# Kernel optimization log

Measured on AMD Instinct MI355X. Metric: run time of the kernel, lower is better.

Reference implementation:

```python
import jax, jax.numpy as jnp
from jax import lax
import numpy as np

IN_F, CELL, OUT_F = 1024, 1024, 1024
B, T = 128, 256


def setup_inputs() -> dict:
    key = jax.random.key(0)
    ks = jax.random.split(key, 12)
    s_gate = 1.0 / np.sqrt(IN_F + CELL)
    s_cls = 1.0 / np.sqrt(CELL)
    d = {
        "x": jax.random.normal(ks[0], (B, T, IN_F), jnp.float32),
        "Wf": jax.random.normal(ks[1], (CELL + IN_F, CELL), jnp.float32) * s_gate,
        "bf": jax.random.normal(ks[2], (CELL,), jnp.float32) * s_gate,
        "Wi1": jax.random.normal(ks[3], (CELL + IN_F, CELL), jnp.float32) * s_gate,
        "bi1": jax.random.normal(ks[4], (CELL,), jnp.float32) * s_gate,
        "Wi2": jax.random.normal(ks[5], (CELL + IN_F, CELL), jnp.float32) * s_gate,
        "bi2": jax.random.normal(ks[6], (CELL,), jnp.float32) * s_gate,
        "Wo": jax.random.normal(ks[7], (CELL + IN_F, CELL), jnp.float32) * s_gate,
        "bo": jax.random.normal(ks[8], (CELL,), jnp.float32) * s_gate,
        "Wc": jax.random.normal(ks[9], (CELL, OUT_F), jnp.float32) * s_cls,
        "bc": jax.random.normal(ks[10], (OUT_F,), jnp.float32) * s_cls,
    }
    return d


def reference(x, Wf, bf, Wi1, bi1, Wi2, bi2, Wo, bo, Wc, bc):
    # x: [B, T, IN_F]
    Bsz, Tlen, _ = x.shape
    H = Wf.shape[1]
    xt = jnp.transpose(x, (1, 0, 2))  # [T, B, IN_F], matches x.permute(1,0,2)

    def step(cell, x_i):
        # concat order matches torch.cat((cell_state, x[i]), dim=2)
        inp = jnp.concatenate([cell, x_i], axis=-1)  # [B, H + IN_F]
        f = jax.nn.sigmoid(inp @ Wf + bf)
        cell1 = cell * f
        i1 = jax.nn.sigmoid(inp @ Wi1 + bi1)
        i2 = jnp.tanh(inp @ Wi2 + bi2)
        cell2 = cell1 + i1 * i2
        o1 = jax.nn.sigmoid(inp @ Wo + bo)
        h = o1 * jnp.tanh(cell2)
        out = h @ Wc + bc  # [B, OUT_F]
        return cell2, out

    c0 = jnp.zeros((Bsz, H), x.dtype)
    c_final, outs = lax.scan(step, c0, xt)  # outs: [T, B, OUT_F]
    output_sequence = jnp.transpose(outs, (1, 0, 2))  # [B, T, OUT_F]
    return output_sequence, c_final[None, :, :]  # cell_state kept as [1, B, H]
```

## Files before the change

### kernel.cpp

```cpp
#include <hip/hip_runtime.h>
#include <cstdint>
#include <cstddef>

#define DEVINL __device__ __forceinline__

typedef __attribute__((ext_vector_type(8))) short bf16x8;
typedef __attribute__((ext_vector_type(4))) float f32x4;
typedef __attribute__((ext_vector_type(4))) unsigned short u16x4;
typedef __attribute__((ext_vector_type(4))) unsigned int u32x4;

static constexpr size_t OFF_XB   = 0;
static constexpr size_t OFF_WHT  = OFF_XB  + (size_t)32768*1024*2;
static constexpr size_t OFF_WXT  = OFF_WHT + (size_t)4096*1024*2;
static constexpr size_t OFF_WCT  = OFF_WXT + (size_t)4096*1024*2;
static constexpr size_t OFF_BIAS = OFF_WCT + (size_t)1024*1024*2;
static constexpr size_t OFF_XW   = OFF_BIAS + 4096*4;
static constexpr size_t OFF_H    = OFF_XW  + (size_t)32768*4096*2;
static constexpr size_t OFF_CB   = OFF_H   + (size_t)32768*1024*2;
static constexpr size_t OFF_BAR  = OFF_CB  + (size_t)2*128*1024*2;
static constexpr size_t WS_NEEDED = OFF_BAR + 32768;

DEVINL unsigned short f2b(float f) {
  union { float f; unsigned u; } v; v.f = f;
  unsigned r = (v.u + 0x7FFFu + ((v.u >> 16) & 1u)) >> 16;
  return (unsigned short)r;
}
DEVINL float b2f(unsigned short h) {
  union { unsigned u; float f; } v; v.u = ((unsigned)h) << 16;
  return v.f;
}
DEVINL float sigmoidf_(float x) { return 1.0f / (1.0f + __expf(-x)); }
DEVINL float tanhf_(float x) { float e = __expf(2.0f * x); return 1.0f - 2.0f / (e + 1.0f); }
DEVINL f32x4 MFMA(bf16x8 a, bf16x8 b, f32x4 c) {
  return __builtin_amdgcn_mfma_f32_16x16x32_bf16(a, b, c, 0, 0, 0);
}
DEVINL void gload16(const void* g, void* l) {
  __builtin_amdgcn_global_load_lds(
      (const __attribute__((address_space(1))) void*)g,
      (__attribute__((address_space(3))) void*)l, 16, 0, 0);
}

__global__ void cvt_x_kernel(const float* __restrict__ x, unsigned short* __restrict__ xb) {
  size_t i = ((size_t)blockIdx.x * 256 + threadIdx.x) * 4;
  float4 v = *(const float4*)(x + i);
  u16x4 o; o.x = f2b(v.x); o.y = f2b(v.y); o.z = f2b(v.z); o.w = f2b(v.w);
  *(u16x4*)(xb + i) = o;
}

__global__ __launch_bounds__(256)
void cvt_w_kernel(const float* __restrict__ Wf, const float* __restrict__ Wi1,
                  const float* __restrict__ Wi2, const float* __restrict__ Wo,
                  unsigned short* __restrict__ WhT, unsigned short* __restrict__ WxT) {
  __shared__ float tile[64][65];
  const int bid = blockIdx.x;
  const int g  = bid & 3;
  const int kt = (bid >> 2) & 15;
  const int jt = bid >> 6;
  const float* W = (g == 0) ? Wf : (g == 1) ? Wi1 : (g == 2) ? Wi2 : Wo;
  const int tid = threadIdx.x;
  const int jj  = tid & 63;
  const int kr  = tid >> 6;

  for (int h = 0; h < 2; ++h) {
    const float* Wb = W + (size_t)(h ? 1024 : 0) * 1024;
#pragma unroll
    for (int i = 0; i < 16; ++i) {
      int kl = i * 4 + kr;
      tile[kl][jj] = Wb[(size_t)(kt * 64 + kl) * 1024 + jt * 64 + jj];
    }
    __syncthreads();
    unsigned short* Out = h ? WxT : WhT;
    unsigned short* op  = Out + (size_t)(4 * (jt * 64 + jj) + g) * 1024 + kt * 64 + kr * 16;
#pragma unroll
    for (int q = 0; q < 4; ++q) {
      u16x4 v;
#pragma unroll
      for (int e = 0; e < 4; ++e)
        ((unsigned short*)&v)[e] = f2b(tile[kr * 16 + q * 4 + e][jj]);
      *(u16x4*)(op + q * 4) = v;
    }
    __syncthreads();
  }
}

__global__ void bias_kernel(const float* __restrict__ bf_, const float* __restrict__ bi1,
                            const float* __restrict__ bi2, const float* __restrict__ bo,
                            float* __restrict__ biasAll) {
  int gc = blockIdx.x * 256 + threadIdx.x;
  int j = gc >> 2, g = gc & 3;
  const float* bb = (g == 0) ? bf_ : (g == 1) ? bi1 : (g == 2) ? bi2 : bo;
  biasAll[gc] = bb[j];
}

__global__ void cvt_wc_kernel(const float* __restrict__ Wc, unsigned short* __restrict__ WcT) {
  int idx = blockIdx.x * 256 + threadIdx.x;
  int k = idx & 1023, n = idx >> 10;
  WcT[idx] = f2b(Wc[(size_t)k * 1024 + n]);
}

template<bool OUT_F32>
__global__ __launch_bounds__(512, 2)
void gemm_bt(const unsigned short* __restrict__ A,
             const unsigned short* __restrict__ Bt,
             const float* __restrict__ bias,
             void* __restrict__ C,
             int M, int N, int K) {
  __shared__ char sT[4][32768];
  const int tid  = threadIdx.x;
  const int lane = tid & 63;
  const int wid  = tid >> 6;
  const int wm   = (wid >> 2) * 128;
  const int wn   = (wid & 3) * 64;

  const int nwg = gridDim.x * gridDim.y;
  const int lin = blockIdx.y * gridDim.x + blockIdx.x;
  const int cpx = nwg >> 3;
  const int swz = (lin & 7) * cpx + (lin >> 3);
  const int m0  = (swz / gridDim.x) * 256;
  const int n0  = (swz % gridDim.x) * 256;

  const int nt = K >> 5;

  f32x4 acc[8][4];
#pragma unroll
  for (int i = 0; i < 8; ++i)
#pragma unroll
    for (int j = 0; j < 4; ++j) acc[i][j] = (f32x4){0.f, 0.f, 0.f, 0.f};

  auto stageA = [&](int kt, int buf) {
#pragma unroll
    for (int l = 0; l < 2; ++l) {
      int s = l * 512 + tid;
      int r = s >> 2, c = s & 3;
      int cg = c ^ ((r >> 1) & 3);
      gload16(A + (size_t)(m0 + r) * K + kt * 32 + cg * 8, sT[buf] + s * 16);
    }
  };
  auto stageB = [&](int kt, int buf) {
#pragma unroll
    for (int l = 0; l < 2; ++l) {
      int s = l * 512 + tid;
      int r = s >> 2, c = s & 3;
      int cg = c ^ ((r >> 1) & 3);
      gload16(Bt + (size_t)(n0 + r) * K + kt * 32 + cg * 8, sT[buf] + 16384 + s * 16);
    }
  };

  stageA(0, 0); stageB(0, 0);
  stageA(1, 1); stageB(1, 1);
  stageA(2, 2); stageB(2, 2);
  asm volatile("s_waitcnt vmcnt(8)" ::: "memory");
  __builtin_amdgcn_s_barrier();

  const int ch = lane >> 4;

#pragma unroll 1
  for (int g = 0; g < nt; ++g) {
    const int rb = g & 3;
    const char* ab = sT[rb];
    const char* bb = sT[rb] + 16384;

    bf16x8 bv[4], av[4];
#pragma unroll
    for (int ni = 0; ni < 4; ++ni) {
      int col = wn + ni * 16 + (lane & 15);
      bv[ni] = *(const bf16x8*)(bb + col * 64 + ((ch ^ ((col >> 1) & 3)) << 4));
    }
#pragma unroll
    for (int mi = 0; mi < 4; ++mi) {
      int row = wm + mi * 16 + (lane & 15);
      av[mi] = *(const bf16x8*)(ab + row * 64 + ((ch ^ ((row >> 1) & 3)) << 4));
    }
    if (g + 3 < nt) stageA(g + 3, (g + 3) & 3);
    __builtin_amdgcn_s_barrier();
    __builtin_amdgcn_s_setprio(1);
#pragma unroll
    for (int mi = 0; mi < 4; ++mi)
#pragma unroll
      for (int ni = 0; ni < 4; ++ni)
        acc[mi][ni] = MFMA(av[mi], bv[ni], acc[mi][ni]);
    __builtin_amdgcn_s_setprio(0);
    __builtin_amdgcn_s_barrier();

#pragma unroll
    for (int mi = 0; mi < 4; ++mi) {
      int row = wm + 64 + mi * 16 + (lane & 15);
      av[mi] = *(const bf16x8*)(ab + row * 64 + ((ch ^ ((row >> 1) & 3)) << 4));
    }
    if (g + 3 < nt) stageB(g + 3, (g + 3) & 3);
    __builtin_amdgcn_s_barrier();
    __builtin_amdgcn_s_setprio(1);
#pragma unroll
    for (int mi = 0; mi < 4; ++mi)
#pragma unroll
      for (int ni = 0; ni < 4; ++ni)
        acc[mi + 4][ni] = MFMA(av[mi], bv[ni], acc[mi + 4][ni]);
    __builtin_amdgcn_s_setprio(0);

    if (g <= nt - 4)      asm volatile("s_waitcnt vmcnt(8)" ::: "memory");
    else if (g == nt - 3) asm volatile("s_waitcnt vmcnt(4)" ::: "memory");
    else if (g == nt - 2) asm volatile("s_waitcnt vmcnt(0)" ::: "memory");
    __builtin_amdgcn_s_barrier();
  }

#pragma unroll
  for (int mi = 0; mi < 8; ++mi)
#pragma unroll
    for (int ni = 0; ni < 4; ++ni)
#pragma unroll
      for (int r = 0; r < 4; ++r) {
        int row = m0 + wm + mi * 16 + (lane >> 4) * 4 + r;
        int col = n0 + wn + ni * 16 + (lane & 15);
        float v = acc[mi][ni][r] + bias[col];
        if (OUT_F32) ((float*)C)[(size_t)row * N + col] = v;
        else ((unsigned short*)C)[(size_t)row * N + col] = f2b(v);
      }
}

__global__ __launch_bounds__(512, 2)
void lstm_persist(const unsigned short* __restrict__ WhT,
                  const unsigned short* __restrict__ XW,
                  unsigned short* __restrict__ H,
                  unsigned short* __restrict__ cB0,
                  unsigned short* __restrict__ cB1,
                  float* __restrict__ cellOut,
                  unsigned* __restrict__ bar) {
  __shared__ __align__(16) char  sA[16 * 2064];
  __shared__ __align__(16) float sP[16 * 132];

  const int tid  = threadIdx.x;
  const int lane = tid & 63;
  const int nh   = tid >> 6;
  const int wgid = blockIdx.x;
  const int mq   = wgid & 7;
  const int cs   = wgid >> 3;
  const int sg   = cs >> 2;

  unsigned* qc   = bar + mq * 64;
  unsigned* qf   = bar + 512 + mq * 64;
  unsigned* gcnt = bar + 1024 + (mq * 8 + sg) * 64;

  const int r0 = lane & 15;
  const int ch = lane >> 4;

  bf16x8 bfr[32];
  {
    const unsigned short* bp = WhT + (size_t)(cs * 128 + nh * 16 + r0) * 1024 + ch * 8;
#pragma unroll
    for (int ks = 0; ks < 32; ++ks)
      bfr[ks] = *(const volatile bf16x8*)(bp + ks * 32);
  }

  const int erow  = tid >> 5;
  const int ecol  = tid & 31;
  const int browg = mq * 16 + erow;
  float cf = 0.f;

  const unsigned short* xwp = XW + (size_t)browg * 256 * 4096 + cs * 128 + ecol * 4;
  unsigned* c0p = (unsigned*)(cB0 + (size_t)browg * 1024 + cs * 32 + ecol);
  unsigned* c1p = (unsigned*)(cB1 + (size_t)browg * 1024 + cs * 32 + ecol);
  unsigned* hp  = (unsigned*)(H + (size_t)browg * 256 * 1024 + cs * 32 + ecol);

  const int strow = tid >> 7;
  const int stcc  = tid & 127;

  u16x4 xw = *(const u16x4*)(xwp);

  for (int t = 0; t < 256; ++t) {
    const unsigned short* cinq = ((t & 1) ? cB1 : cB0) + (size_t)mq * 16 * 1024;

    u32x4 st[4];
#pragma unroll
    for (int it = 0; it < 4; ++it) {
      const void* p = cinq + (size_t)(it * 4 + strow) * 1024 + stcc * 8;
      asm volatile("global_load_dwordx4 %0, %1, off sc0 sc1"
                   : "=&v"(st[it]) : "v"(p) : "memory");
    }
    asm volatile("s_waitcnt vmcnt(0)" ::: "memory");
    __builtin_amdgcn_sched_barrier(0);
#pragma unroll
    for (int it = 0; it < 4; ++it) {
      int r = it * 4 + strow;
      *(u32x4*)&sA[r * 2064 + stcc * 16] = st[it];
    }
    __syncthreads();

    f32x4 acc = (f32x4){0.f, 0.f, 0.f, 0.f};
#pragma unroll
    for (int ks = 0; ks < 32; ++ks) {
      bf16x8 a0 = *(const bf16x8*)&sA[r0 * 2064 + (ch + ks * 4) * 16];
      acc = MFMA(a0, bfr[ks], acc);
    }

#pragma unroll
    for (int rr = 0; rr < 4; ++rr)
      sP[(ch * 4 + rr) * 132 + nh * 16 + r0] = acc[rr];
    __syncthreads();

    float4 g = *(const float4*)&sP[erow * 132 + ecol * 4];
    float pf = g.x + b2f((unsigned short)xw[0]);
    float pi = g.y + b2f((unsigned short)xw[1]);
    float pg = g.z + b2f((unsigned short)xw[2]);
    float f  = sigmoidf_(pf), i1 = sigmoidf_(pi), gg = tanhf_(pg);
    float c2 = cf * f + i1 * gg; cf = c2;

    unsigned cl = f2b(c2);
    unsigned chi = __shfl_down(cl, 1);
    if (!(lane & 1))
      __hip_atomic_store((t & 1) ? c0p : c1p, cl | (chi << 16),
                         __ATOMIC_RELAXED, __HIP_MEMORY_SCOPE_AGENT);

    __syncthreads();
    if (tid == 0) {
      unsigned tgt1 = 4u * (unsigned)(t + 1);
      unsigned tgt2 = 8u * (unsigned)(t + 1);
      unsigned n = __hip_atomic_fetch_add(gcnt, 1u, __ATOMIC_RELAXED,
                                          __HIP_MEMORY_SCOPE_AGENT);
      if (n == tgt1 - 1u) {
        unsigned m = __hip_atomic_fetch_add(qc, 1u, __ATOMIC_RELAXED,
                                            __HIP_MEMORY_SCOPE_AGENT);
        if (m == tgt2 - 1u)
          __hip_atomic_store(qf, (unsigned)(t + 1),
                             __ATOMIC_RELAXED, __HIP_MEMORY_SCOPE_AGENT);
      }
    }

    {
      float po = g.w + b2f((unsigned short)xw[3]);
      float h  = sigmoidf_(po) * tanhf_(c2);
      unsigned hl = f2b(h);
      unsigned hh = __shfl_down(hl, 1);
      if (!(lane & 1))
        *(hp + (size_t)t * 512) = hl | (hh << 16);
    }
    if (t < 255) xw = *(const u16x4*)(xwp + (size_t)(t + 1) * 4096);

    if (tid == 0) {
      while (__hip_atomic_load(qf, __ATOMIC_RELAXED, __HIP_MEMORY_SCOPE_AGENT)
             < (unsigned)(t + 1))
        __builtin_amdgcn_s_sleep(1);
    }
    __syncthreads();
  }

  cellOut[(size_t)browg * 1024 + cs * 32 + ecol] = cf;
}

extern "C" void kernel_launch(void* const* d_in, const int* in_sizes, int n_in,
                              void* d_out, int out_size, void* d_ws, size_t ws_size,
                              hipStream_t stream) {
  const float* x   = (const float*)d_in[0];
  const float* Wf  = (const float*)d_in[1];
  const float* bfv = (const float*)d_in[2];
  const float* Wi1 = (const float*)d_in[3];
  const float* bi1 = (const float*)d_in[4];
  const float* Wi2 = (const float*)d_in[5];
  const float* bi2 = (const float*)d_in[6];
  const float* Wo  = (const float*)d_in[7];
  const float* bo  = (const float*)d_in[8];
  const float* Wc  = (const float*)d_in[9];
  const float* bc  = (const float*)d_in[10];
  float* out = (float*)d_out;

  if (ws_size < WS_NEEDED) return;

  char* ws = (char*)d_ws;
  unsigned short* xb      = (unsigned short*)(ws + OFF_XB);
  unsigned short* WhT     = (unsigned short*)(ws + OFF_WHT);
  unsigned short* WxT     = (unsigned short*)(ws + OFF_WXT);
  unsigned short* WcT     = (unsigned short*)(ws + OFF_WCT);
  float*          biasAll = (float*)(ws + OFF_BIAS);
  unsigned short* XW      = (unsigned short*)(ws + OFF_XW);
  unsigned short* H       = (unsigned short*)(ws + OFF_H);
  unsigned short* cB0     = (unsigned short*)(ws + OFF_CB);
  unsigned short* cB1     = (unsigned short*)(ws + OFF_CB + (size_t)128 * 1024 * 2);
  unsigned*       barLn   = (unsigned*)(ws + OFF_BAR);
  float*          cellOut = out + (size_t)32768 * 1024;

  hipMemsetAsync(cB0, 0, (size_t)128 * 1024 * 2, stream);
  hipMemsetAsync(barLn, 0, 32768, stream);

  cvt_x_kernel <<<32768, 256, 0, stream>>>(x, xb);
  cvt_w_kernel <<< 1024, 256, 0, stream>>>(Wf, Wi1, Wi2, Wo, WhT, WxT);
  bias_kernel  <<<   16, 256, 0, stream>>>(bfv, bi1, bi2, bo, biasAll);
  cvt_wc_kernel<<< 4096, 256, 0, stream>>>(Wc, WcT);

  gemm_bt<false><<<dim3(16, 128), 512, 0, stream>>>(xb, WxT, biasAll, XW, 32768, 4096, 1024);

  {
    void* args[] = { (void*)&WhT, (void*)&XW, (void*)&H,
                     (void*)&cB0, (void*)&cB1, (void*)&cellOut, (void*)&barLn };
    hipLaunchCooperativeKernel(lstm_persist, dim3(256), dim3(512), args, 0u, stream);
  }

  gemm_bt<true><<<dim3(4, 128), 512, 0, stream>>>(H, WcT, bc, out, 32768, 1024, 1024);
}
```

Before: 1.337 ms.

## Replace LDS gate transpose with in-register quad shuffles and split MFMA accumulators

The persistent recurrent kernel no longer writes MFMA gate results to shared memory and re-reads them after a barrier. Instead, each thread redistributes the four gate pre-activations inside its quad using lane shuffles, with thread-to-cell mapping changed to match. This removes one __syncthreads and the LDS round-trip from every timestep of the serial critical path. The MFMA chain is also split into four independent accumulators to break the dependency chain. In exchange it adds select/shuffle instructions and changes the h/c store pattern to stride-4 lane pairing.

```diff
diff --git a/kernel.cpp b/kernel.cpp
--- a/kernel.cpp
+++ b/kernel.cpp
@@ -225,8 +225,7 @@
                   unsigned short* __restrict__ cB1,
                   float* __restrict__ cellOut,
                   unsigned* __restrict__ bar) {
-  __shared__ __align__(16) char  sA[16 * 2064];
-  __shared__ __align__(16) float sP[16 * 132];
+  __shared__ __align__(16) char sA[16 * 2064];
 
   const int tid  = threadIdx.x;
   const int lane = tid & 63;
@@ -242,6 +241,8 @@
 
   const int r0 = lane & 15;
   const int ch = lane >> 4;
+  const int qq = r0 >> 2;
+  const int g  = r0 & 3;
 
   bf16x8 bfr[32];
   {
@@ -251,15 +252,14 @@
       bfr[ks] = *(const volatile bf16x8*)(bp + ks * 32);
   }
 
-  const int erow  = tid >> 5;
-  const int ecol  = tid & 31;
-  const int browg = mq * 16 + erow;
+  const int browg = mq * 16 + ch * 4 + g;
+  const int ccol  = cs * 32 + nh * 4 + qq;
   float cf = 0.f;
 
-  const unsigned short* xwp = XW + (size_t)browg * 256 * 4096 + cs * 128 + ecol * 4;
-  unsigned* c0p = (unsigned*)(cB0 + (size_t)browg * 1024 + cs * 32 + ecol);
-  unsigned* c1p = (unsigned*)(cB1 + (size_t)browg * 1024 + cs * 32 + ecol);
-  unsigned* hp  = (unsigned*)(H + (size_t)browg * 256 * 1024 + cs * 32 + ecol);
+  const unsigned short* xwp = XW + (size_t)browg * 256 * 4096 + ccol * 4;
+  unsigned* c0p = (unsigned*)(cB0 + (size_t)browg * 1024 + ccol);
+  unsigned* c1p = (unsigned*)(cB1 + (size_t)browg * 1024 + ccol);
+  unsigned* hp  = (unsigned*)(H + (size_t)browg * 256 * 1024 + ccol);
 
   const int strow = tid >> 7;
   const int stcc  = tid & 127;
@@ -285,28 +285,42 @@
     }
     __syncthreads();
 
-    f32x4 acc = (f32x4){0.f, 0.f, 0.f, 0.f};
-#pragma unroll
-    for (int ks = 0; ks < 32; ++ks) {
-      bf16x8 a0 = *(const bf16x8*)&sA[r0 * 2064 + (ch + ks * 4) * 16];
-      acc = MFMA(a0, bfr[ks], acc);
-    }
-
-#pragma unroll
-    for (int rr = 0; rr < 4; ++rr)
-      sP[(ch * 4 + rr) * 132 + nh * 16 + r0] = acc[rr];
-    __syncthreads();
-
-    float4 g = *(const float4*)&sP[erow * 132 + ecol * 4];
-    float pf = g.x + b2f((unsigned short)xw[0]);
-    float pi = g.y + b2f((unsigned short)xw[1]);
-    float pg = g.z + b2f((unsigned short)xw[2]);
-    float f  = sigmoidf_(pf), i1 = sigmoidf_(pi), gg = tanhf_(pg);
-    float c2 = cf * f + i1 * gg; cf = c2;
-
-    unsigned cl = f2b(c2);
-    unsigned chi = __shfl_down(cl, 1);
-    if (!(lane & 1))
+    f32x4 aA = (f32x4){0.f, 0.f, 0.f, 0.f};
+    f32x4 aB = (f32x4){0.f, 0.f, 0.f, 0.f};
+    f32x4 aC = (f32x4){0.f, 0.f, 0.f, 0.f};
+    f32x4 aD = (f32x4){0.f, 0.f, 0.f, 0.f};
+#pragma unroll
+    for (int ks = 0; ks < 32; ks += 4) {
+      aA = MFMA(*(const bf16x8*)&sA[r0 * 2064 + (ch + ks * 4) * 16],       bfr[ks],     aA);
+      aB = MFMA(*(const bf16x8*)&sA[r0 * 2064 + (ch + (ks + 1) * 4) * 16], bfr[ks + 1], aB);
+      aC = MFMA(*(const bf16x8*)&sA[r0 * 2064 + (ch + (ks + 2) * 4) * 16], bfr[ks + 2], aC);
+      aD = MFMA(*(const bf16x8*)&sA[r0 * 2064 + (ch + (ks + 3) * 4) * 16], bfr[ks + 3], aD);
+    }
+    f32x4 acc = (aA + aB) + (aC + aD);
+
+    float a0 = acc[0], a1 = acc[1], a2 = acc[2], a3 = acc[3];
+    float v0 = (g == 0) ? a0 : (g == 1) ? a1 : (g == 2) ? a2 : a3;
+    float p1 = (g == 0) ? a3 : (g == 1) ? a0 : (g == 2) ? a1 : a2;
+    float p2 = (g == 0) ? a2 : (g == 1) ? a3 : (g == 2) ? a0 : a1;
+    float p3 = (g == 0) ? a1 : (g == 1) ? a2 : (g == 2) ? a3 : a0;
+    const int qb = lane & ~3;
+    float v1 = __shfl(p1, qb | ((g + 1) & 3));
+    float v2 = __shfl(p2, qb | ((g + 2) & 3));
+    float v3 = __shfl(p3, qb | ((g + 3) & 3));
+    float pf = (g == 0) ? v0 : (g == 1) ? v3 : (g == 2) ? v2 : v1;
+    float pi = (g == 0) ? v1 : (g == 1) ? v0 : (g == 2) ? v3 : v2;
+    float pg = (g == 0) ? v2 : (g == 1) ? v1 : (g == 2) ? v0 : v3;
+    float po = (g == 0) ? v3 : (g == 1) ? v2 : (g == 2) ? v1 : v0;
+
+    pf += b2f((unsigned short)xw[0]);
+    pi += b2f((unsigned short)xw[1]);
+    pg += b2f((unsigned short)xw[2]);
+    float f  = sigmoidf_(pf), i1 = sigmoidf_(pi), gg2 = tanhf_(pg);
+    float c2 = cf * f + i1 * gg2; cf = c2;
+
+    unsigned cl  = f2b(c2);
+    unsigned chi = __shfl_down(cl, 4);
+    if (!(qq & 1))
       __hip_atomic_store((t & 1) ? c0p : c1p, cl | (chi << 16),
                          __ATOMIC_RELAXED, __HIP_MEMORY_SCOPE_AGENT);
 
@@ -326,11 +340,11 @@
     }
 
     {
-      float po = g.w + b2f((unsigned short)xw[3]);
-      float h  = sigmoidf_(po) * tanhf_(c2);
+      float poa = po + b2f((unsigned short)xw[3]);
+      float h   = sigmoidf_(poa) * tanhf_(c2);
       unsigned hl = f2b(h);
-      unsigned hh = __shfl_down(hl, 1);
-      if (!(lane & 1))
+      unsigned hh = __shfl_down(hl, 4);
+      if (!(qq & 1))
         *(hp + (size_t)t * 512) = hl | (hh << 16);
     }
     if (t < 255) xw = *(const u16x4*)(xwp + (size_t)(t + 1) * 4096);
@@ -343,7 +357,7 @@
     __syncthreads();
   }
 
-  cellOut[(size_t)browg * 1024 + cs * 32 + ecol] = cf;
+  cellOut[(size_t)browg * 1024 + ccol] = cf;
 }
 
 extern "C" void kernel_launch(void* const* d_in, const int* in_sizes, int n_in,
```

Result: slower. 1.382 ms (+3.4%).
